# Optimization experiments

Hardware: AMD Instinct MI355X
Metric: run time of the kernel (lower is better)

Reference implementation:

```python
import jax, jax.numpy as jnp
import numpy as np

N_NODES = 50000
N_EDGES = 1_600_000
REL_NUM = 16
D_IN = 64
D_OUT = 64


def setup_inputs() -> dict:
    key = jax.random.key(0)
    k_h, k_w, k_n, k_s, k_d, k_r = jax.random.split(key, 6)
    h = jax.random.normal(k_h, (N_NODES, D_IN), dtype=jnp.float32)
    # xavier_uniform over (rel_num, input_dim, output_dim): fan_in=input_dim, fan_out=output_dim
    limit = float(np.sqrt(6.0 / (D_IN + D_OUT)))
    weight = jax.random.uniform(k_w, (REL_NUM, D_IN, D_OUT), dtype=jnp.float32,
                                minval=-limit, maxval=limit)
    norm = jax.random.uniform(k_n, (N_EDGES, 1), dtype=jnp.float32)
    src = jax.random.randint(k_s, (N_EDGES,), 0, N_NODES)
    dst = jax.random.randint(k_d, (N_EDGES,), 0, N_NODES)
    rel_type = jax.random.randint(k_r, (N_EDGES,), 0, REL_NUM)
    return {"h": h, "weight": weight, "norm": norm,
            "src": src, "dst": dst, "rel_type": rel_type}


def reference(h, weight, norm, src, dst, rel_type):
    # Non-input path of R_GCN_Layer:
    #   msg_e = (h[src_e] @ weight[rel_e]) * norm_e ; h'_v = relu(sum_{e->v} msg_e)
    # Instead of gathering a [E, D_in, D_out] weight tensor per edge (huge),
    # transform every node by every relation once, then gather per (src, rel).
    n_nodes = h.shape[0]
    transformed = jnp.einsum('nd,rdo->nro', h, weight)      # [N, R, D_out]
    msg = transformed[src, rel_type] * norm                  # [E, D_out]
    agg = jax.ops.segment_sum(msg, dst, num_segments=n_nodes)  # [N, D_out]
    return jax.nn.relu(agg)
```

## Files before the change

kernel.cpp:

```cpp
#include <hip/hip_runtime.h>
#include <hip/hip_bf16.h>

#define N_NODES 50000
#define N_EDGES 1600000
#define NREL    16
#define DIM     64

#define NTILE   3125

#define CB_SH   7
#define NCB     391
#define P1_CHUNK 2048
#define P1_GRID  782

#define CB_R_ARENA 5120
#define LBIN    6080
#define PREP_HBLK 3125

typedef __attribute__((ext_vector_type(8))) short short8;
typedef __attribute__((ext_vector_type(4))) float float4v;
typedef __attribute__((ext_vector_type(4))) unsigned short ushort4v;

template<int IS_F32>
__device__ __forceinline__ float ldx(const void* p, size_t i) {
    if (IS_F32) {
        return ((const float*)p)[i];
    } else {
        unsigned short u = ((const unsigned short*)p)[i];
        return __uint_as_float(((unsigned)u) << 16);
    }
}

__device__ __forceinline__ float bfbits2f(unsigned short u) {
    return __uint_as_float(((unsigned)u) << 16);
}

__device__ __forceinline__ unsigned short f2bfbits(float v) {
    __hip_bfloat16 b = __float2bfloat16(v);
    unsigned short us; __builtin_memcpy(&us, &b, 2);
    return us;
}

__global__ __launch_bounds__(1024) void k_detect(
    const float* __restrict__ norm_f, int* __restrict__ flag,
    int* __restrict__ gcur)
{
    __shared__ int sbad;
    if (threadIdx.x == 0) sbad = 0;
    if (threadIdx.x < NCB) gcur[threadIdx.x] = 0;
    __syncthreads();
    float v = norm_f[threadIdx.x];
    int bad = (v != v || fabsf(v) > 1e3f) ? 1 : 0;
    if (bad) atomicOr(&sbad, 1);
    __syncthreads();
    if (threadIdx.x == 0) *flag = sbad ? 0 : 1;
}

template<int IS_F32>
__device__ __forceinline__ void split_body(
    const int* __restrict__ src, const int* __restrict__ dst,
    const int* __restrict__ rel, const void* __restrict__ norm_raw,
    int* __restrict__ gcur, unsigned long long* __restrict__ R,
    int* hist, int* curs)
{
    const int blk = blockIdx.x;
    for (int i = threadIdx.x; i < NCB; i += 256) hist[i] = 0;
    __syncthreads();
    const int e0 = blk * P1_CHUNK;
    for (int i = threadIdx.x; i < P1_CHUNK; i += 256) {
        int e = e0 + i;
        if (e < N_EDGES) atomicAdd(&hist[dst[e] >> CB_SH], 1);
    }
    __syncthreads();
    for (int b = threadIdx.x; b < NCB; b += 256) {
        int c = hist[b];
        if (c > 0) {
            int s = atomicAdd(&gcur[b], c);
            if (s + c > CB_R_ARENA) s = CB_R_ARENA - c;
            curs[b] = b * CB_R_ARENA + s;
        }
    }
    __syncthreads();
    for (int i = threadIdx.x; i < P1_CHUNK; i += 256) {
        int e = e0 + i;
        if (e >= N_EDGES) continue;
        int d = dst[e];
        int pos = atomicAdd(&curs[d >> CB_SH], 1);
        unsigned short nb = f2bfbits(ldx<IS_F32>(norm_raw, e));
        unsigned long long rec =
              (unsigned long long)(d & 127)
            | ((unsigned long long)(unsigned)src[e] << 8)
            | ((unsigned long long)(unsigned)rel[e] << 24)
            | ((unsigned long long)nb << 32);
        R[pos] = rec;
    }
}

__global__ __launch_bounds__(256) void k_split_prep(
    const int* __restrict__ src, const int* __restrict__ dst,
    const int* __restrict__ rel, const void* __restrict__ norm_raw,
    int* __restrict__ gcur, unsigned long long* __restrict__ R,
    const void* __restrict__ h_raw, const void* __restrict__ w_raw,
    unsigned short* __restrict__ hbf, unsigned short* __restrict__ Wswz,
    const int* __restrict__ flag)
{
    __shared__ int hist[NCB];
    __shared__ int curs[NCB];
    const int blk = blockIdx.x;
    if (blk < P1_GRID) {
        if (*flag) split_body<1>(src, dst, rel, norm_raw, gcur, R, hist, curs);
        else       split_body<0>(src, dst, rel, norm_raw, gcur, R, hist, curs);
    } else {
        const int f = *flag;
        const int blk2 = blk - P1_GRID;
        if (blk2 < PREP_HBLK) {
            const int x = threadIdx.x & 15, rl = threadIdx.x >> 4;
            const int row = blk2 * 16 + rl;
            const size_t rb = (size_t)row * 64;
            ushort4v o;
            if (f) {
                const float* hf = (const float*)h_raw;
                o[0] = f2bfbits(hf[rb + x]);
                o[1] = f2bfbits(hf[rb + x + 16]);
                o[2] = f2bfbits(hf[rb + x + 32]);
                o[3] = f2bfbits(hf[rb + x + 48]);
            } else {
                const unsigned short* hr = (const unsigned short*)h_raw;
                o[0] = hr[rb + x];
                o[1] = hr[rb + x + 16];
                o[2] = hr[rb + x + 32];
                o[3] = hr[rb + x + 48];
            }
            *(ushort4v*)(hbf + rb + 4 * x) = o;
        } else {
            int rel2 = blk2 - PREP_HBLK;
            for (int idx = threadIdx.x; idx < 4096; idx += 256) {
                int d = idx >> 6, o = idx & 63;
                float wv = f ? ((const float*)w_raw)[(size_t)((rel2 << 6) + d) * 64 + o]
                             : bfbits2f(((const unsigned short*)w_raw)[(size_t)((rel2 << 6) + d) * 64 + o]);
                int c = d >> 5, q = (d >> 3) & 3, j = d & 7;
                Wswz[(size_t)rel2 * 5120 + ((c << 6) + o) * 40 + q * 8 + j] = f2bfbits(wv);
            }
        }
    }
}

#define MFMA_BF16 __builtin_amdgcn_mfma_f32_16x16x32_bf16

__global__ __launch_bounds__(512) void k_fuse3(
    const int* __restrict__ gcur,
    const unsigned long long* __restrict__ R,
    const unsigned short* __restrict__ hbf,
    const unsigned short* __restrict__ Wswz,
    void* __restrict__ out, const int* __restrict__ flag)
{
    __shared__ unsigned pkL[LBIN];
    __shared__ unsigned short nrmL[LBIN];
    __shared__ int cnt[128], sbl[128], cur[128];
    __shared__ int tot0s;
    __shared__ __align__(16) unsigned short sbuf[8][16 * 72];

    const int tid = threadIdx.x, cb = blockIdx.x;
    const int wave = tid >> 6, lane = tid & 63;
    const int n15 = lane & 15, quad = lane >> 4;

    if (tid < 128) { cnt[tid] = 0; cur[tid] = 0; }
    __syncthreads();

    const int c0  = cb * CB_R_ARENA;
    const int run = min(gcur[cb], CB_R_ARENA);

    for (int i = tid; i < run; i += 512) {
        unsigned long long rec = R[c0 + i];
        int bin = (int)((rec >> 24) & 15) * 8 + (int)((rec >> 4) & 7);
        atomicAdd(&cnt[bin], 1);
    }
    __syncthreads();

    if (tid < 64) {
        int c = (cnt[tid] + 7) & ~7, incl = c;
#pragma unroll
        for (int off = 1; off < 64; off <<= 1) {
            int t = __shfl_up(incl, off, 64);
            if (tid >= off) incl += t;
        }
        sbl[tid] = incl - c;
        if (tid == 63) tot0s = incl;
    }
    __syncthreads();
    if (tid >= 64 && tid < 128) {
        int l2 = tid - 64;
        int c = (cnt[tid] + 7) & ~7, incl = c;
#pragma unroll
        for (int off = 1; off < 64; off <<= 1) {
            int t = __shfl_up(incl, off, 64);
            if (l2 >= off) incl += t;
        }
        sbl[tid] = tot0s + incl - c;
    }
    __syncthreads();

    for (int i = tid; i < run; i += 512) {
        unsigned long long rec = R[c0 + i];
        int bin = (int)((rec >> 24) & 15) * 8 + (int)((rec >> 4) & 7);
        int pos = sbl[bin] + atomicAdd(&cur[bin], 1);
        pkL[pos]  = (unsigned)rec & 0x00FFFF0Fu;
        nrmL[pos] = (unsigned short)(rec >> 32);
    }
    __syncthreads();

    const int tile = cb * 8 + wave;

    float4v ac0 = {0.f,0.f,0.f,0.f}, ac1 = {0.f,0.f,0.f,0.f};
    float4v ac2 = {0.f,0.f,0.f,0.f}, ac3 = {0.f,0.f,0.f,0.f};
    unsigned short* sb_ = &sbuf[wave][0];

    for (int r = 0; r < NREL; ++r) {
        const int bin = r * 8 + wave;
        const int bb = sbl[bin], bc = cnt[bin];
        if (bc == 0) continue;
        const int nch = (bc + 31) >> 5;

        float4v s0 = {0.f,0.f,0.f,0.f}, s1 = {0.f,0.f,0.f,0.f};
        float4v s2 = {0.f,0.f,0.f,0.f}, s3 = {0.f,0.f,0.f,0.f};

        for (int c = 0; c < nch; ++c) {
            const int base = bb + (c << 5) + (quad << 3);
            const int rem  = bc - ((c << 5) + (quad << 3));
            const uint4 pa = *(const uint4*)&pkL[base];
            const uint4 pb = *(const uint4*)&pkL[base + 4];
            const ushort4v na = *(const ushort4v*)&nrmL[base];
            const ushort4v nb = *(const ushort4v*)&nrmL[base + 4];

            const unsigned r0s = (rem > 0) ? (pa.x >> 8) : 0u;
            const unsigned r1s = (rem > 1) ? (pa.y >> 8) : 0u;
            const unsigned r2s = (rem > 2) ? (pa.z >> 8) : 0u;
            const unsigned r3s = (rem > 3) ? (pa.w >> 8) : 0u;
            const unsigned r4s = (rem > 4) ? (pb.x >> 8) : 0u;
            const unsigned r5s = (rem > 5) ? (pb.y >> 8) : 0u;
            const unsigned r6s = (rem > 6) ? (pb.z >> 8) : 0u;
            const unsigned r7s = (rem > 7) ? (pb.w >> 8) : 0u;

            const int co = 4 * n15;
            ushort4v v0 = *(const ushort4v*)(hbf + (size_t)r0s * 64 + co);
            ushort4v v1 = *(const ushort4v*)(hbf + (size_t)r1s * 64 + co);
            ushort4v v2 = *(const ushort4v*)(hbf + (size_t)r2s * 64 + co);
            ushort4v v3 = *(const ushort4v*)(hbf + (size_t)r3s * 64 + co);
            ushort4v v4 = *(const ushort4v*)(hbf + (size_t)r4s * 64 + co);
            ushort4v v5 = *(const ushort4v*)(hbf + (size_t)r5s * 64 + co);
            ushort4v v6 = *(const ushort4v*)(hbf + (size_t)r6s * 64 + co);
            ushort4v v7 = *(const ushort4v*)(hbf + (size_t)r7s * 64 + co);

            short8 av;
            av[0] = (rem > 0 && (int)(pa.x & 15u) == n15) ? (short)na[0] : (short)0;
            av[1] = (rem > 1 && (int)(pa.y & 15u) == n15) ? (short)na[1] : (short)0;
            av[2] = (rem > 2 && (int)(pa.z & 15u) == n15) ? (short)na[2] : (short)0;
            av[3] = (rem > 3 && (int)(pa.w & 15u) == n15) ? (short)na[3] : (short)0;
            av[4] = (rem > 4 && (int)(pb.x & 15u) == n15) ? (short)nb[0] : (short)0;
            av[5] = (rem > 5 && (int)(pb.y & 15u) == n15) ? (short)nb[1] : (short)0;
            av[6] = (rem > 6 && (int)(pb.z & 15u) == n15) ? (short)nb[2] : (short)0;
            av[7] = (rem > 7 && (int)(pb.w & 15u) == n15) ? (short)nb[3] : (short)0;

#define BV_MFMA(S, K) \
            { short8 bv; \
              bv[0] = (short)v0[K]; bv[1] = (short)v1[K]; \
              bv[2] = (short)v2[K]; bv[3] = (short)v3[K]; \
              bv[4] = (short)v4[K]; bv[5] = (short)v5[K]; \
              bv[6] = (short)v6[K]; bv[7] = (short)v7[K]; \
              S = MFMA_BF16(av, bv, S, 0, 0, 0); }

            BV_MFMA(s0, 0)
            BV_MFMA(s1, 1)
            BV_MFMA(s2, 2)
            BV_MFMA(s3, 3)
#undef BV_MFMA
        }

#pragma unroll
        for (int i = 0; i < 4; ++i) {
            sb_[(quad * 4 + i) * 72 +  0 + n15] = f2bfbits(s0[i]);
            sb_[(quad * 4 + i) * 72 + 16 + n15] = f2bfbits(s1[i]);
            sb_[(quad * 4 + i) * 72 + 32 + n15] = f2bfbits(s2[i]);
            sb_[(quad * 4 + i) * 72 + 48 + n15] = f2bfbits(s3[i]);
        }

        const short8 a0 = *(const short8*)(sb_ + n15 * 72 + quad * 8);
        const short8 a1 = *(const short8*)(sb_ + n15 * 72 + 32 + quad * 8);

        const unsigned short* wp = Wswz + (size_t)r * 5120;
        const short8 w00 = *(const short8*)(wp + ( 0 + n15) * 40 + quad * 8);
        const short8 w01 = *(const short8*)(wp + (16 + n15) * 40 + quad * 8);
        const short8 w02 = *(const short8*)(wp + (32 + n15) * 40 + quad * 8);
        const short8 w03 = *(const short8*)(wp + (48 + n15) * 40 + quad * 8);
        const short8 w10 = *(const short8*)(wp + (64 + n15) * 40 + quad * 8);
        const short8 w11 = *(const short8*)(wp + (80 + n15) * 40 + quad * 8);
        const short8 w12 = *(const short8*)(wp + (96 + n15) * 40 + quad * 8);
        const short8 w13 = *(const short8*)(wp + (112 + n15) * 40 + quad * 8);

        ac0 = MFMA_BF16(a0, w00, ac0, 0, 0, 0);
        ac1 = MFMA_BF16(a0, w01, ac1, 0, 0, 0);
        ac2 = MFMA_BF16(a0, w02, ac2, 0, 0, 0);
        ac3 = MFMA_BF16(a0, w03, ac3, 0, 0, 0);
        ac0 = MFMA_BF16(a1, w10, ac0, 0, 0, 0);
        ac1 = MFMA_BF16(a1, w11, ac1, 0, 0, 0);
        ac2 = MFMA_BF16(a1, w12, ac2, 0, 0, 0);
        ac3 = MFMA_BF16(a1, w13, ac3, 0, 0, 0);
    }

    if (tile < NTILE) {
        const int node0 = tile << 4;
        const int f = *flag;
#define STORE_T(AC, T) \
        { \
            _Pragma("unroll") \
            for (int i = 0; i < 4; ++i) { \
                float rv = fmaxf(AC[i], 0.f); \
                size_t ob = (size_t)(node0 + quad * 4 + i) * 64 + (T) * 16 + n15; \
                if (f) ((float*)out)[ob] = rv; \
                else   ((unsigned short*)out)[ob] = f2bfbits(rv); \
            } \
        }
        STORE_T(ac0, 0)
        STORE_T(ac1, 1)
        STORE_T(ac2, 2)
        STORE_T(ac3, 3)
#undef STORE_T
    }
}

extern "C" void kernel_launch(void* const* d_in, const int* in_sizes, int n_in,
                              void* d_out, int out_size, void* d_ws, size_t ws_size,
                              hipStream_t stream)
{
    const void* h      = d_in[0];
    const void* weight = d_in[1];
    const void* norm   = d_in[2];
    const int* src = (const int*)d_in[3];
    const int* dst = (const int*)d_in[4];
    const int* rel = (const int*)d_in[5];

    char* w = (char*)d_ws;
    int* flag = (int*)w;                        w += 256;
    int* gcur = (int*)w;                        w += (NCB * 4 + 255) / 256 * 256;
    unsigned long long* R = (unsigned long long*)w;  w += (size_t)NCB * CB_R_ARENA * 8;
    unsigned short* hbf = (unsigned short*)w;   w += (size_t)N_NODES * DIM * 2;
    unsigned short* Wswz = (unsigned short*)w;  w += (size_t)NREL * 5120 * 2;

    k_detect<<<1, 1024, 0, stream>>>((const float*)norm, flag, gcur);

    k_split_prep<<<P1_GRID + PREP_HBLK + NREL, 256, 0, stream>>>(
        src, dst, rel, norm, gcur, R, h, weight, hbf, Wswz, flag);

    k_fuse3<<<NCB, 512, 0, stream>>>(gcur, R, hbf, Wswz, d_out, flag);
}
```

Before: 180.3 us.

## Stage binned edge records in LDS for coalesced scatter to global bins

The split phase now sorts each block's edge records by coarse destination bin inside a shared-memory staging buffer, using a wave-level prefix scan over the local histogram. It then writes them to the global arena in contiguous runs instead of scattering each record individually. dst values are kept in registers to avoid reloading them. This trades scattered 8-byte global writes for coalesced ones, at the cost of 16KB+ of extra LDS per block (lower occupancy) and extra barriers.

```diff
diff --git a/kernel.cpp b/kernel.cpp
--- a/kernel.cpp
+++ b/kernel.cpp
@@ -61,38 +61,76 @@
     const int* __restrict__ src, const int* __restrict__ dst,
     const int* __restrict__ rel, const void* __restrict__ norm_raw,
     int* __restrict__ gcur, unsigned long long* __restrict__ R,
-    int* hist, int* curs)
+    unsigned long long* stage, int* hist, int* lstart, int* gstart,
+    int* lcur, int* totS)
 {
     const int blk = blockIdx.x;
-    for (int i = threadIdx.x; i < NCB; i += 256) hist[i] = 0;
-    __syncthreads();
+    const int tid = threadIdx.x;
+    for (int i = tid; i < NCB; i += 256) { hist[i] = 0; lcur[i] = 0; }
+    __syncthreads();
+
     const int e0 = blk * P1_CHUNK;
-    for (int i = threadIdx.x; i < P1_CHUNK; i += 256) {
-        int e = e0 + i;
-        if (e < N_EDGES) atomicAdd(&hist[dst[e] >> CB_SH], 1);
-    }
-    __syncthreads();
-    for (int b = threadIdx.x; b < NCB; b += 256) {
+    int dreg[8];
+#pragma unroll
+    for (int k = 0; k < 8; ++k) {
+        int e = e0 + k * 256 + tid;
+        int d = (e < N_EDGES) ? dst[e] : -1;
+        dreg[k] = d;
+        if (d >= 0) atomicAdd(&hist[d >> CB_SH], 1);
+    }
+    __syncthreads();
+
+    if (tid < 64) {
+        int carry = 0;
+        for (int chunk = 0; chunk < (NCB + 63) / 64; ++chunk) {
+            int i = chunk * 64 + tid;
+            int c = (i < NCB) ? hist[i] : 0;
+            int incl = c;
+#pragma unroll
+            for (int off = 1; off < 64; off <<= 1) {
+                int t = __shfl_up(incl, off, 64);
+                if (tid >= off) incl += t;
+            }
+            if (i < NCB) lstart[i] = carry + incl - c;
+            carry += __shfl(incl, 63, 64);
+        }
+        if (tid == 0) *totS = carry;
+    }
+    __syncthreads();
+
+    for (int b = tid; b < NCB; b += 256) {
         int c = hist[b];
         if (c > 0) {
             int s = atomicAdd(&gcur[b], c);
             if (s + c > CB_R_ARENA) s = CB_R_ARENA - c;
-            curs[b] = b * CB_R_ARENA + s;
-        }
-    }
-    __syncthreads();
-    for (int i = threadIdx.x; i < P1_CHUNK; i += 256) {
-        int e = e0 + i;
-        if (e >= N_EDGES) continue;
-        int d = dst[e];
-        int pos = atomicAdd(&curs[d >> CB_SH], 1);
+            gstart[b] = b * CB_R_ARENA + s;
+        }
+    }
+    __syncthreads();
+
+#pragma unroll
+    for (int k = 0; k < 8; ++k) {
+        int e = e0 + k * 256 + tid;
+        int d = dreg[k];
+        if (d < 0) continue;
+        int cb = d >> CB_SH;
+        int pos = lstart[cb] + atomicAdd(&lcur[cb], 1);
         unsigned short nb = f2bfbits(ldx<IS_F32>(norm_raw, e));
         unsigned long long rec =
               (unsigned long long)(d & 127)
             | ((unsigned long long)(unsigned)src[e] << 8)
             | ((unsigned long long)(unsigned)rel[e] << 24)
-            | ((unsigned long long)nb << 32);
-        R[pos] = rec;
+            | ((unsigned long long)nb << 32)
+            | ((unsigned long long)(unsigned)cb << 48);
+        stage[pos] = rec;
+    }
+    __syncthreads();
+
+    const int tot = *totS;
+    for (int i = tid; i < tot; i += 256) {
+        unsigned long long rec = stage[i];
+        int bin = (int)((rec >> 48) & 511u);
+        R[gstart[bin] + (i - lstart[bin])] = rec;
     }
 }
 
@@ -104,12 +142,15 @@
     unsigned short* __restrict__ hbf, unsigned short* __restrict__ Wswz,
     const int* __restrict__ flag)
 {
-    __shared__ int hist[NCB];
-    __shared__ int curs[NCB];
+    __shared__ unsigned long long stage[P1_CHUNK];
+    __shared__ int hist[NCB], lstart[NCB], gstart[NCB], lcur[NCB];
+    __shared__ int totS;
     const int blk = blockIdx.x;
     if (blk < P1_GRID) {
-        if (*flag) split_body<1>(src, dst, rel, norm_raw, gcur, R, hist, curs);
-        else       split_body<0>(src, dst, rel, norm_raw, gcur, R, hist, curs);
+        if (*flag) split_body<1>(src, dst, rel, norm_raw, gcur, R,
+                                 stage, hist, lstart, gstart, lcur, &totS);
+        else       split_body<0>(src, dst, rel, norm_raw, gcur, R,
+                                 stage, hist, lstart, gstart, lcur, &totS);
     } else {
         const int f = *flag;
         const int blk2 = blk - P1_GRID;
```

After: 171.7 us (median of 2 runs). 1.05x faster.
